# Optimization experiments

Measured on AMD Instinct MI355X. Metric: run time of the kernel, lower is better.

The kernel has to match this reference:

```python
import jax, jax.numpy as jnp
import numpy as np

N = 100000      # num vertices
M = 100000      # num hyperedges
NNZ = 800000    # incidence pairs
IN_CH = 128
H, C = 8, 16    # heads, out_channels
NEG_SLOPE = 0.2


def setup_inputs() -> dict:
    key = jax.random.key(0)
    k1, k2, k3, k4, k5 = jax.random.split(key, 5)
    X = jax.random.normal(k1, (N, IN_CH), dtype=jnp.float32)
    vertex = jax.random.randint(k2, (NNZ,), 0, N, dtype=jnp.int32)
    edges = jax.random.randint(k3, (NNZ,), 0, M, dtype=jnp.int32)
    # glorot init: Linear W (in, H*C) and att_e (1, H, C)
    std_w = float(np.sqrt(6.0 / (IN_CH + H * C)))
    W = jax.random.uniform(k4, (IN_CH, H * C), minval=-std_w, maxval=std_w, dtype=jnp.float32)
    std_a = float(np.sqrt(6.0 / (H + C)))
    att_e = jax.random.uniform(k5, (1, H, C), minval=-std_a, maxval=std_a, dtype=jnp.float32)
    return {"X": X, "W": W, "att_e": att_e, "vertex": vertex, "edges": edges}


def reference(X, W, att_e, vertex, edges):
    Nn = X.shape[0]
    nnz = vertex.shape[0]
    # X0 = self.W(X)  -> (N, H*C), then view (N, H, C)
    X0 = X @ W
    Xh = X0.reshape(Nn, H, C)
    # gather per incidence, mean-aggregate to hyperedges (first_aggregate='mean')
    Xve = Xh[vertex]                                            # (nnz, H, C)
    e_sum = jax.ops.segment_sum(Xve, edges, num_segments=M)     # (M, H, C)
    e_cnt = jax.ops.segment_sum(jnp.ones((nnz,), X.dtype), edges, num_segments=M)
    Xe = e_sum / jnp.maximum(e_cnt, 1.0)[:, None, None]
    # edge attention logits
    alpha_e = (Xe * att_e).sum(-1)                              # (M, H)
    a = alpha_e[edges]                                          # (nnz, H)
    a = jnp.where(a >= 0, a, NEG_SLOPE * a)                     # leaky_relu
    # segment softmax over incidences grouped by destination vertex
    amax = jax.ops.segment_max(a, vertex, num_segments=Nn)      # (N, H)
    amax = jnp.where(jnp.isfinite(amax), amax, 0.0)
    ex = jnp.exp(a - amax[vertex])
    denom = jax.ops.segment_sum(ex, vertex, num_segments=Nn)
    alpha = ex / (denom[vertex] + 1e-16)                        # (nnz, H)
    # attention-weighted scatter-sum back to vertices
    Xev = Xe[edges] * alpha[:, :, None]                         # (nnz, H, C)
    Xv = jax.ops.segment_sum(Xev, vertex, num_segments=Nn)      # (N, H, C)
    return Xv.reshape(Nn, H * C)
```

## Files before the change

kernel.cpp:

```cpp
#include <hip/hip_runtime.h>
#include <hip/hip_bf16.h>

#define N_V   100000
#define N_E   100000
#define NNZ_C 800000
#define HC    128
#define H_    8
#define C_    16
#define NEG   0.2f
#define BSH   9
#define KPB   512
#define NBUCK 196
#define CAP   5120
#define CHUNK 4096
#define GEMM_NB ((N_V + 63) / 64)

typedef __attribute__((ext_vector_type(8))) short bf16x8;
typedef __attribute__((ext_vector_type(4))) float f32x4;
typedef unsigned long long ull;

__device__ __forceinline__ short f2bf(float f) {
    unsigned u = __float_as_uint(f);
    unsigned r = (u + 0x7FFFu + ((u >> 16) & 1u)) >> 16;
    return (short)r;
}
__device__ __forceinline__ float bf2f(unsigned short u) {
    return __uint_as_float(((unsigned)u) << 16);
}
__device__ __forceinline__ unsigned pack2(float lo, float hi) {
    return ((unsigned)(unsigned short)f2bf(hi) << 16) | (unsigned short)f2bf(lo);
}
__device__ __forceinline__ void acc8w(float* acc, uint4 p, float wt) {
    acc[0] += __uint_as_float(p.x << 16) * wt;
    acc[1] += __uint_as_float(p.x & 0xFFFF0000u) * wt;
    acc[2] += __uint_as_float(p.y << 16) * wt;
    acc[3] += __uint_as_float(p.y & 0xFFFF0000u) * wt;
    acc[4] += __uint_as_float(p.z << 16) * wt;
    acc[5] += __uint_as_float(p.z & 0xFFFF0000u) * wt;
    acc[6] += __uint_as_float(p.w << 16) * wt;
    acc[7] += __uint_as_float(p.w & 0xFFFF0000u) * wt;
}
__device__ __forceinline__ void acc8(float* acc, uint4 p) {
    acc[0] += __uint_as_float(p.x << 16);
    acc[1] += __uint_as_float(p.x & 0xFFFF0000u);
    acc[2] += __uint_as_float(p.y << 16);
    acc[3] += __uint_as_float(p.y & 0xFFFF0000u);
    acc[4] += __uint_as_float(p.z << 16);
    acc[5] += __uint_as_float(p.z & 0xFFFF0000u);
    acc[6] += __uint_as_float(p.w << 16);
    acc[7] += __uint_as_float(p.w & 0xFFFF0000u);
}

__global__ __launch_bounds__(256) void wt_k(const float* __restrict__ W, unsigned short* __restrict__ Wt) {
    int i = blockIdx.x * 256 + threadIdx.x;
    int k = i >> 7, c = i & 127;
    Wt[c * 128 + k] = (unsigned short)f2bf(W[k * 128 + c]);
}

__global__ __launch_bounds__(256) void fusedA_k(const float* __restrict__ X,
                                                const unsigned short* __restrict__ Wt,
                                                unsigned short* __restrict__ X0b,
                                                const int* __restrict__ edges,
                                                const int* __restrict__ vertex,
                                                int* __restrict__ bcur_e, int* __restrict__ bcur_v,
                                                unsigned* __restrict__ stage_e, unsigned* __restrict__ stage_v) {
    __shared__ union {
        unsigned long long wlds[4096];
        struct { int he[NBUCK]; int hv[NBUCK]; } h;
    } sm;
    int tid = threadIdx.x;

    if (blockIdx.x >= NBUCK) {
        int blk = blockIdx.x - NBUCK;
        const unsigned long long* wt8 = (const unsigned long long*)Wt;
        for (int u = tid; u < 4096; u += 256) {
            int col = u >> 5, g = u & 31;
            sm.wlds[(col << 5) | (g ^ (col & 15))] = wt8[u];
        }
        __syncthreads();

        int wave = tid >> 6, lane = tid & 63;
        int cl = lane & 15, kq = lane >> 4;
        int base = blk * 64 + wave * 16;
        int rowA = base + cl;
        int srcRow = (rowA < N_V) ? rowA : (N_V - 1);

        f32x4 acc[8] = {};
        const float4* X4 = (const float4*)X;

        #pragma unroll
        for (int ks = 0; ks < 4; ++ks) {
            float4 a0 = X4[(size_t)srcRow * 32 + 8 * ks + kq];
            float4 a1 = X4[(size_t)srcRow * 32 + 8 * ks + 4 + kq];
            bf16x8 af;
            af[0] = f2bf(a0.x); af[1] = f2bf(a0.y); af[2] = f2bf(a0.z); af[3] = f2bf(a0.w);
            af[4] = f2bf(a1.x); af[5] = f2bf(a1.y); af[6] = f2bf(a1.z); af[7] = f2bf(a1.w);
            int g0 = 8 * ks + kq;
            int g1 = g0 + 4;
            #pragma unroll
            for (int ct = 0; ct < 8; ++ct) {
                int col = ct * 16 + cl;
                union { unsigned long long q[2]; bf16x8 v; } bu;
                bu.q[0] = sm.wlds[(col << 5) | (g0 ^ cl)];
                bu.q[1] = sm.wlds[(col << 5) | (g1 ^ cl)];
                acc[ct] = __builtin_amdgcn_mfma_f32_16x16x32_bf16(af, bu.v, acc[ct], 0, 0, 0);
            }
        }
        int rbase = base + kq * 4;
        #pragma unroll
        for (int ct = 0; ct < 8; ++ct) {
            #pragma unroll
            for (int r = 0; r < 4; ++r) {
                int row = rbase + r;
                if (row < N_V) X0b[(size_t)row * 128 + ct * 16 + cl] = (unsigned short)f2bf(acc[ct][r]);
            }
        }
    } else {
        for (int i = tid; i < NBUCK; i += 256) { sm.h.he[i] = 0; sm.h.hv[i] = 0; }
        __syncthreads();
        int e0 = blockIdx.x * CHUNK;
        int e1 = e0 + CHUNK; if (e1 > NNZ_C) e1 = NNZ_C;
        for (int i = e0 + tid; i < e1; i += 256) {
            atomicAdd(&sm.h.he[edges[i] >> BSH], 1);
            atomicAdd(&sm.h.hv[vertex[i] >> BSH], 1);
        }
        __syncthreads();
        for (int i = tid; i < NBUCK; i += 256) {
            int c = sm.h.he[i]; sm.h.he[i] = c ? atomicAdd(&bcur_e[i], c) : 0;
            c = sm.h.hv[i];     sm.h.hv[i] = c ? atomicAdd(&bcur_v[i], c) : 0;
        }
        __syncthreads();
        for (int i = e0 + tid; i < e1; i += 256) {
            int ed = edges[i], v = vertex[i];
            int be = ed >> BSH, bv = v >> BSH;
            int pe = atomicAdd(&sm.h.he[be], 1);
            stage_e[(size_t)be * CAP + pe] = ((unsigned)(ed & (KPB - 1)) << 17) | (unsigned)v;
            int pv = atomicAdd(&sm.h.hv[bv], 1);
            stage_v[(size_t)bv * CAP + pv] = ((unsigned)(v & (KPB - 1)) << 17) | (unsigned)ed;
        }
    }
}

__global__ __launch_bounds__(512) void bsort_k(const unsigned* __restrict__ stage_e,
                                               const unsigned* __restrict__ stage_v,
                                               const int* __restrict__ bcur_e, const int* __restrict__ bcur_v,
                                               int* __restrict__ e_off, int* __restrict__ v_off,
                                               int* __restrict__ e_idx, int* __restrict__ v_idx) {
    bool isE = blockIdx.x < NBUCK;
    int b = isE ? blockIdx.x : blockIdx.x - NBUCK;
    const unsigned* stage = (isE ? stage_e : stage_v) + (size_t)b * CAP;
    const int* bcnt = isE ? bcur_e : bcur_v;
    int* off = isE ? e_off : v_off;
    int* idx = isE ? e_idx : v_idx;
    int t = threadIdx.x;

    __shared__ int sb[256];
    __shared__ int cntk[KPB];
    __shared__ int loc[KPB];
    if (t < 256) sb[t] = (t < NBUCK) ? bcnt[t] : 0;
    cntk[t] = 0;
    __syncthreads();
    for (int dd = 1; dd < 256; dd <<= 1) {
        int v = (t < 256 && t >= dd) ? sb[t - dd] : 0;
        __syncthreads();
        if (t < 256 && t >= dd) sb[t] += v;
        __syncthreads();
    }
    int cnt = bcnt[b];
    int bbase = sb[b] - cnt;

    for (int i = t; i < cnt; i += 512)
        atomicAdd(&cntk[stage[i] >> 17], 1);
    __syncthreads();
    int val = cntk[t];
    loc[t] = val;
    __syncthreads();
    for (int dd = 1; dd < 512; dd <<= 1) {
        int tv = (t >= dd) ? loc[t - dd] : 0;
        __syncthreads();
        loc[t] += tv;
        __syncthreads();
    }
    int pos0 = bbase + loc[t] - val;
    int key = (b << BSH) + t;
    if (key < N_V) off[key] = pos0;
    cntk[t] = pos0;
    __syncthreads();
    for (int i = t; i < cnt; i += 512) {
        unsigned p = stage[i];
        int pos = atomicAdd(&cntk[p >> 17], 1);
        idx[pos] = (int)(p & 0x1FFFF);
    }
    if (blockIdx.x == 0 && t == 0) { e_off[N_E] = NNZ_C; v_off[N_V] = NNZ_C; }
}

__global__ __launch_bounds__(256) void agg_gather_k(const uint4* __restrict__ X0b4,
                                                    const int* __restrict__ e_off,
                                                    const int* __restrict__ e_idx,
                                                    const float* __restrict__ att,
                                                    uint4* __restrict__ Xeb4,
                                                    float* __restrict__ alpha_l) {
    int wave = (int)((blockIdx.x * 256 + threadIdx.x) >> 6);
    int lane = threadIdx.x & 63;
    if (wave >= N_E) return;
    int beg = e_off[wave], end = e_off[wave + 1];
    int deg = end - beg;
    int j = lane & 15, g = lane >> 4;

    float acc[8] = {0.f, 0.f, 0.f, 0.f, 0.f, 0.f, 0.f, 0.f};
    const uint4 Z = {0u, 0u, 0u, 0u};

    if (deg <= 64) {
        int vl = (lane < deg) ? e_idx[beg + lane] : 0;
        for (int r0 = 0; r0 < deg; r0 += 16) {
            int r_0 = r0 + g, r_1 = r0 + 4 + g, r_2 = r0 + 8 + g, r_3 = r0 + 12 + g;
            int v_0 = __shfl(vl, r_0), v_1 = __shfl(vl, r_1);
            int v_2 = __shfl(vl, r_2), v_3 = __shfl(vl, r_3);
            uint4 p_0 = Z, p_1 = Z, p_2 = Z, p_3 = Z;
            if (r_0 < deg) p_0 = X0b4[(size_t)v_0 * 16 + j];
            if (r_1 < deg) p_1 = X0b4[(size_t)v_1 * 16 + j];
            if (r_2 < deg) p_2 = X0b4[(size_t)v_2 * 16 + j];
            if (r_3 < deg) p_3 = X0b4[(size_t)v_3 * 16 + j];
            acc8(acc, p_0); acc8(acc, p_1); acc8(acc, p_2); acc8(acc, p_3);
        }
    } else {
        for (int i0 = beg; i0 < end; i0 += 4) {
            int i = i0 + g;
            uint4 p = Z;
            if (i < end) p = X0b4[(size_t)e_idx[i] * 16 + j];
            acc8(acc, p);
        }
    }
    #pragma unroll
    for (int k = 0; k < 8; ++k) {
        acc[k] += __shfl_xor(acc[k], 16);
        acc[k] += __shfl_xor(acc[k], 32);
    }
    float inv = 1.f / fmaxf((float)deg, 1.f);
    uint4 o;
    o.x = pack2(acc[0] * inv, acc[1] * inv);
    o.y = pack2(acc[2] * inv, acc[3] * inv);
    o.z = pack2(acc[4] * inv, acc[5] * inv);
    o.w = pack2(acc[6] * inv, acc[7] * inv);
    if (g == 0) Xeb4[(size_t)wave * 16 + j] = o;

    const float4* att4 = (const float4*)att;
    float4 A0 = att4[2 * j], A1 = att4[2 * j + 1];
    float s = bf2f((unsigned short)(o.x & 0xFFFF)) * A0.x + bf2f((unsigned short)(o.x >> 16)) * A0.y
            + bf2f((unsigned short)(o.y & 0xFFFF)) * A0.z + bf2f((unsigned short)(o.y >> 16)) * A0.w
            + bf2f((unsigned short)(o.z & 0xFFFF)) * A1.x + bf2f((unsigned short)(o.z >> 16)) * A1.y
            + bf2f((unsigned short)(o.w & 0xFFFF)) * A1.z + bf2f((unsigned short)(o.w >> 16)) * A1.w;
    s += __shfl_xor(s, 1);
    if (g == 0 && (j & 1) == 0) {
        s = (s >= 0.f) ? s : NEG * s;
        alpha_l[wave * 8 + (j >> 1)] = s;
    }
}

__global__ __launch_bounds__(256) void out_fused_k(const uint4* __restrict__ Xeb4,
                                                   const float* __restrict__ alpha_l,
                                                   const int* __restrict__ v_off,
                                                   const int* __restrict__ v_idx,
                                                   float* __restrict__ out) {
    int wave = (int)((blockIdx.x * 256 + threadIdx.x) >> 6);
    int lane = threadIdx.x & 63;
    if (wave >= N_V) return;
    int beg = v_off[wave], end = v_off[wave + 1];
    int deg = end - beg;
    int j = lane & 15, g = lane >> 4, h = j >> 1;

    float acc[8] = {0.f, 0.f, 0.f, 0.f, 0.f, 0.f, 0.f, 0.f};
    float d = 0.f;
    const uint4 Z = {0u, 0u, 0u, 0u};

    if (deg <= 64) {
        int vl = (lane < deg) ? v_idx[beg + lane] : 0;
        for (int r0 = 0; r0 < deg; r0 += 16) {
            int r_0 = r0 + g, r_1 = r0 + 4 + g, r_2 = r0 + 8 + g, r_3 = r0 + 12 + g;
            int e_0 = __shfl(vl, r_0), e_1 = __shfl(vl, r_1);
            int e_2 = __shfl(vl, r_2), e_3 = __shfl(vl, r_3);
            bool b_0 = r_0 < deg, b_1 = r_1 < deg, b_2 = r_2 < deg, b_3 = r_3 < deg;
            float a_0 = 0.f, a_1 = 0.f, a_2 = 0.f, a_3 = 0.f;
            uint4 p_0 = Z, p_1 = Z, p_2 = Z, p_3 = Z;
            if (b_0) { a_0 = alpha_l[e_0 * 8 + h]; p_0 = Xeb4[(size_t)e_0 * 16 + j]; }
            if (b_1) { a_1 = alpha_l[e_1 * 8 + h]; p_1 = Xeb4[(size_t)e_1 * 16 + j]; }
            if (b_2) { a_2 = alpha_l[e_2 * 8 + h]; p_2 = Xeb4[(size_t)e_2 * 16 + j]; }
            if (b_3) { a_3 = alpha_l[e_3 * 8 + h]; p_3 = Xeb4[(size_t)e_3 * 16 + j]; }
            float w_0 = b_0 ? __expf(a_0) : 0.f;
            float w_1 = b_1 ? __expf(a_1) : 0.f;
            float w_2 = b_2 ? __expf(a_2) : 0.f;
            float w_3 = b_3 ? __expf(a_3) : 0.f;
            d += w_0 + w_1 + w_2 + w_3;
            acc8w(acc, p_0, w_0); acc8w(acc, p_1, w_1);
            acc8w(acc, p_2, w_2); acc8w(acc, p_3, w_3);
        }
    } else {
        for (int i0 = beg; i0 < end; i0 += 4) {
            int i = i0 + g;
            float w = 0.f;
            uint4 p = Z;
            if (i < end) {
                int ed = v_idx[i];
                w = __expf(alpha_l[ed * 8 + h]);
                p = Xeb4[(size_t)ed * 16 + j];
            }
            d += w;
            acc8w(acc, p, w);
        }
    }
    d += __shfl_xor(d, 16);
    d += __shfl_xor(d, 32);
    float rd = 1.f / (d + 1e-16f);
    #pragma unroll
    for (int k = 0; k < 8; ++k) {
        acc[k] += __shfl_xor(acc[k], 16);
        acc[k] += __shfl_xor(acc[k], 32);
        acc[k] *= rd;
    }
    if (g == 0) {
        float4* out4 = (float4*)out;
        float4 o0 = {acc[0], acc[1], acc[2], acc[3]};
        float4 o1 = {acc[4], acc[5], acc[6], acc[7]};
        out4[(size_t)wave * 32 + 2 * j]     = o0;
        out4[(size_t)wave * 32 + 2 * j + 1] = o1;
    }
}

extern "C" void kernel_launch(void* const* d_in, const int* in_sizes, int n_in,
                              void* d_out, int out_size, void* d_ws, size_t ws_size,
                              hipStream_t stream) {
    const float* X      = (const float*)d_in[0];
    const float* W      = (const float*)d_in[1];
    const float* att    = (const float*)d_in[2];
    const int*   vertex = (const int*)d_in[3];
    const int*   edges  = (const int*)d_in[4];
    float* out = (float*)d_out;

    unsigned short* X0b = (unsigned short*)d_ws;
    unsigned short* Xeb = X0b + (size_t)N_V * HC;
    unsigned* stage_e = (unsigned*)(Xeb + (size_t)N_E * HC);
    unsigned* stage_v = stage_e + (size_t)NBUCK * CAP;
    int*   e_off   = (int*)(stage_v + (size_t)NBUCK * CAP);
    int*   v_off   = e_off + (N_E + 1);
    int*   e_idx   = v_off + (N_V + 1);
    int*   v_idx   = e_idx + NNZ_C;
    float* alpha_l = (float*)(v_idx + NNZ_C);
    int*   bcur_e  = (int*)(alpha_l + (size_t)N_E * H_);
    int*   bcur_v  = bcur_e + NBUCK;
    unsigned short* Wt = (unsigned short*)(bcur_v + NBUCK);

    hipMemsetAsync(bcur_e, 0, sizeof(int) * 2 * NBUCK, stream);

    wt_k<<<64, 256, 0, stream>>>(W, Wt);

    fusedA_k<<<NBUCK + GEMM_NB, 256, 0, stream>>>(X, Wt, X0b, edges, vertex,
                                                  bcur_e, bcur_v, stage_e, stage_v);

    bsort_k<<<2 * NBUCK, 512, 0, stream>>>(stage_e, stage_v, bcur_e, bcur_v,
                                           e_off, v_off, e_idx, v_idx);

    agg_gather_k<<<(N_E * 64) / 256, 256, 0, stream>>>((const uint4*)X0b, e_off, e_idx, att,
                                                       (uint4*)Xeb, alpha_l);

    out_fused_k<<<(N_V * 64) / 256, 256, 0, stream>>>((const uint4*)Xeb, alpha_l, v_off, v_idx, out);
}
```

Measured before the change: 151.5 us.

## Double GEMM rows per wave and halve scatter chunk size in fused kernel

Each GEMM wave now computes two 16-row tiles that share the same LDS-loaded W fragments, so a block covers 128 rows and the shared-memory B loads are reused across two MFMAs. Separately, the bucket-scatter portion now uses 2048-element chunks, giving 391 scatter blocks instead of 196, which adds parallelism and lowers per-block work. The trade-offs are higher register pressure from two accumulator sets and more global atomics on the bucket cursors from the extra scatter blocks.

```diff
diff --git a/kernel.cpp b/kernel.cpp
--- a/kernel.cpp
+++ b/kernel.cpp
@@ -12,8 +12,9 @@
 #define KPB   512
 #define NBUCK 196
 #define CAP   5120
-#define CHUNK 4096
-#define GEMM_NB ((N_V + 63) / 64)
+#define CHUNK 2048
+#define SCAT_NB ((NNZ_C + CHUNK - 1) / CHUNK)
+#define GEMM_NB ((N_V + 127) / 128)
 
 typedef __attribute__((ext_vector_type(8))) short bf16x8;
 typedef __attribute__((ext_vector_type(4))) float f32x4;
@@ -70,8 +71,8 @@
     } sm;
     int tid = threadIdx.x;
 
-    if (blockIdx.x >= NBUCK) {
-        int blk = blockIdx.x - NBUCK;
+    if (blockIdx.x >= SCAT_NB) {
+        int blk = blockIdx.x - SCAT_NB;
         const unsigned long long* wt8 = (const unsigned long long*)Wt;
         for (int u = tid; u < 4096; u += 256) {
             int col = u >> 5, g = u & 31;
@@ -81,20 +82,26 @@
 
         int wave = tid >> 6, lane = tid & 63;
         int cl = lane & 15, kq = lane >> 4;
-        int base = blk * 64 + wave * 16;
-        int rowA = base + cl;
-        int srcRow = (rowA < N_V) ? rowA : (N_V - 1);
-
-        f32x4 acc[8] = {};
+        int base = blk * 128 + wave * 32;
+        int rowA0 = base + cl;
+        int rowA1 = base + 16 + cl;
+        int src0 = (rowA0 < N_V) ? rowA0 : (N_V - 1);
+        int src1 = (rowA1 < N_V) ? rowA1 : (N_V - 1);
+
+        f32x4 accA[8] = {}, accB[8] = {};
         const float4* X4 = (const float4*)X;
 
         #pragma unroll
         for (int ks = 0; ks < 4; ++ks) {
-            float4 a0 = X4[(size_t)srcRow * 32 + 8 * ks + kq];
-            float4 a1 = X4[(size_t)srcRow * 32 + 8 * ks + 4 + kq];
-            bf16x8 af;
-            af[0] = f2bf(a0.x); af[1] = f2bf(a0.y); af[2] = f2bf(a0.z); af[3] = f2bf(a0.w);
-            af[4] = f2bf(a1.x); af[5] = f2bf(a1.y); af[6] = f2bf(a1.z); af[7] = f2bf(a1.w);
+            float4 a0 = X4[(size_t)src0 * 32 + 8 * ks + kq];
+            float4 a1 = X4[(size_t)src0 * 32 + 8 * ks + 4 + kq];
+            float4 b0 = X4[(size_t)src1 * 32 + 8 * ks + kq];
+            float4 b1 = X4[(size_t)src1 * 32 + 8 * ks + 4 + kq];
+            bf16x8 afA, afB;
+            afA[0] = f2bf(a0.x); afA[1] = f2bf(a0.y); afA[2] = f2bf(a0.z); afA[3] = f2bf(a0.w);
+            afA[4] = f2bf(a1.x); afA[5] = f2bf(a1.y); afA[6] = f2bf(a1.z); afA[7] = f2bf(a1.w);
+            afB[0] = f2bf(b0.x); afB[1] = f2bf(b0.y); afB[2] = f2bf(b0.z); afB[3] = f2bf(b0.w);
+            afB[4] = f2bf(b1.x); afB[5] = f2bf(b1.y); afB[6] = f2bf(b1.z); afB[7] = f2bf(b1.w);
             int g0 = 8 * ks + kq;
             int g1 = g0 + 4;
             #pragma unroll
@@ -103,16 +110,20 @@
                 union { unsigned long long q[2]; bf16x8 v; } bu;
                 bu.q[0] = sm.wlds[(col << 5) | (g0 ^ cl)];
                 bu.q[1] = sm.wlds[(col << 5) | (g1 ^ cl)];
-                acc[ct] = __builtin_amdgcn_mfma_f32_16x16x32_bf16(af, bu.v, acc[ct], 0, 0, 0);
+                accA[ct] = __builtin_amdgcn_mfma_f32_16x16x32_bf16(afA, bu.v, accA[ct], 0, 0, 0);
+                accB[ct] = __builtin_amdgcn_mfma_f32_16x16x32_bf16(afB, bu.v, accB[ct], 0, 0, 0);
             }
         }
-        int rbase = base + kq * 4;
+        int rb0 = base + kq * 4;
+        int rb1 = base + 16 + kq * 4;
         #pragma unroll
         for (int ct = 0; ct < 8; ++ct) {
             #pragma unroll
             for (int r = 0; r < 4; ++r) {
-                int row = rbase + r;
-                if (row < N_V) X0b[(size_t)row * 128 + ct * 16 + cl] = (unsigned short)f2bf(acc[ct][r]);
+                int row0 = rb0 + r;
+                int row1 = rb1 + r;
+                if (row0 < N_V) X0b[(size_t)row0 * 128 + ct * 16 + cl] = (unsigned short)f2bf(accA[ct][r]);
+                if (row1 < N_V) X0b[(size_t)row1 * 128 + ct * 16 + cl] = (unsigned short)f2bf(accB[ct][r]);
             }
         }
     } else {
@@ -353,8 +364,8 @@
 
     wt_k<<<64, 256, 0, stream>>>(W, Wt);
 
-    fusedA_k<<<NBUCK + GEMM_NB, 256, 0, stream>>>(X, Wt, X0b, edges, vertex,
-                                                  bcur_e, bcur_v, stage_e, stage_v);
+    fusedA_k<<<SCAT_NB + GEMM_NB, 256, 0, stream>>>(X, Wt, X0b, edges, vertex,
+                                                    bcur_e, bcur_v, stage_e, stage_v);
 
     bsort_k<<<2 * NBUCK, 512, 0, stream>>>(stage_e, stage_v, bcur_e, bcur_v,
                                            e_off, v_off, e_idx, v_idx);
```

Result: slower. 161.5 us (+6.6%).
